# Kernel tuning notes

Measured on AMD Instinct MI355X. Metric: run time of the kernel, lower is better.

## Reference

```python
import jax, jax.numpy as jnp
import numpy as np

B, S, H = 2, 2048, 2048
E, I, TOPK = 8, 1408, 2


def setup_inputs() -> dict:
    key = jax.random.key(0)
    k0, k1, k2, k3, k4 = jax.random.split(key, 5)
    return {
        "hidden_states": jax.random.normal(k0, (B, S, H), dtype=jnp.float32),
        "Wr": jax.random.normal(k1, (H, E), dtype=jnp.float32) * 0.02,
        "Wg": jax.random.normal(k2, (E, H, I), dtype=jnp.float32) * 0.02,
        "Wu": jax.random.normal(k3, (E, H, I), dtype=jnp.float32) * 0.02,
        "Wd": jax.random.normal(k4, (E, I, H), dtype=jnp.float32) * 0.02,
    }


def reference(hidden_states, Wr, Wg, Wu, Wd):
    b, s, h = hidden_states.shape
    x = hidden_states.reshape(-1, h)                      # [T, H]
    T = x.shape[0]
    router_logits = x @ Wr                                # [T, E]
    probs = jax.nn.softmax(router_logits.astype(jnp.float32), axis=-1)
    top_w, top_i = jax.lax.top_k(probs, TOPK)             # [T, k]
    top_w = top_w / jnp.sum(top_w, axis=-1, keepdims=True)  # norm_topk_prob
    top_w = top_w.astype(x.dtype)
    # combine weights per (token, expert): zero where expert not selected
    cw = jnp.zeros((T, E), dtype=x.dtype).at[
        jnp.arange(T)[:, None], top_i].add(top_w)         # [T, E]
    # per-expert SwiGLU MLP computed densely, masked/weighted by cw
    g = jax.nn.silu(jnp.einsum('th,ehi->tei', x, Wg))     # [T, E, I]
    u = jnp.einsum('th,ehi->tei', x, Wu)                  # [T, E, I]
    y = jnp.einsum('tei,eih->teh', g * u, Wd)             # [T, E, H]
    out = jnp.einsum('te,teh->th', cw, y)                 # [T, H]
    return out.reshape(b, s, h), router_logits
```

## Files before the change

kernel.cpp:

```cpp
#include <hip/hip_runtime.h>

#define T_TOK 4096
#define HD 2048
#define NE 8
#define NI 1408

typedef __bf16 bf16x8 __attribute__((ext_vector_type(8)));
typedef float f32x4 __attribute__((ext_vector_type(4)));
typedef unsigned short ushort8 __attribute__((ext_vector_type(8)));

#define S_WAITCNT_VMCNT(n) asm volatile("s_waitcnt vmcnt(" #n ")" ::: "memory")
__device__ __forceinline__ void wave_barrier() {
  asm volatile("" ::: "memory");
  __builtin_amdgcn_s_barrier();
  asm volatile("" ::: "memory");
}

__device__ __forceinline__ unsigned short f2bf(float f) {
  unsigned int u = __float_as_uint(f);
  u += 0x7FFFu + ((u >> 16) & 1u);
  return (unsigned short)(u >> 16);
}
__device__ __forceinline__ float bf2f(unsigned short u) {
  return __uint_as_float((unsigned int)u << 16);
}

__device__ __forceinline__ void gload_lds16(const void* g, void* l) {
  __builtin_amdgcn_global_load_lds(
      (const __attribute__((address_space(1))) unsigned int*)g,
      (__attribute__((address_space(3))) unsigned int*)l, 16, 0, 0);
}

__global__ void transpose_cvt_kernel(const float* __restrict__ src,
                                     unsigned short* __restrict__ dst,
                                     int R, int C) {
  __shared__ float tile[64][65];
  int e = blockIdx.z;
  int r0 = blockIdx.y * 64, c0 = blockIdx.x * 64;
  const float* s = src + (size_t)e * R * C;
  unsigned short* d = dst + (size_t)e * R * C;
  int tid = threadIdx.x;
  int lr = tid >> 4, lc = (tid & 15) * 4;
#pragma unroll
  for (int p = 0; p < 4; p++) {
    int r = lr + p * 16;
    float4 v = *(const float4*)(s + (size_t)(r0 + r) * C + c0 + lc);
    tile[r][lc] = v.x; tile[r][lc + 1] = v.y;
    tile[r][lc + 2] = v.z; tile[r][lc + 3] = v.w;
  }
  __syncthreads();
  int rbase = (tid & 7) * 8, crel = tid >> 3;
#pragma unroll
  for (int p = 0; p < 2; p++) {
    int c = p * 32 + crel;
    ushort8 o;
#pragma unroll
    for (int j = 0; j < 8; j++) o[j] = f2bf(tile[rbase + j][c]);
    *(ushort8*)(d + (size_t)(c0 + c) * R + r0 + rbase) = o;
  }
}

__global__ void router_kernel(const float* __restrict__ x,
                              const float* __restrict__ Wr,
                              float* __restrict__ logits,
                              unsigned short* __restrict__ xbf,
                              int4* __restrict__ tokinfo,
                              int* __restrict__ cnt) {
  int wv = threadIdx.x >> 6, lane = threadIdx.x & 63;
  int t = blockIdx.x * 4 + wv;
  const float* xr = x + (size_t)t * HD;
  unsigned short* xbr = xbf + (size_t)t * HD;
  float acc[NE];
#pragma unroll
  for (int e = 0; e < NE; e++) acc[e] = 0.f;
  for (int hi = 0; hi < HD / 64; hi++) {
    int h = hi * 64 + lane;
    float xv = xr[h];
    xbr[h] = f2bf(xv);
    const float4* w4 = (const float4*)(Wr + (size_t)h * NE);
    float4 a = w4[0], b = w4[1];
    acc[0] += xv * a.x; acc[1] += xv * a.y; acc[2] += xv * a.z; acc[3] += xv * a.w;
    acc[4] += xv * b.x; acc[5] += xv * b.y; acc[6] += xv * b.z; acc[7] += xv * b.w;
  }
#pragma unroll
  for (int m = 32; m > 0; m >>= 1) {
#pragma unroll
    for (int e = 0; e < NE; e++) acc[e] += __shfl_xor(acc[e], m, 64);
  }
  if (lane < NE) logits[(size_t)t * NE + lane] = acc[lane];
  if (lane == 0) {
    int e0 = 0;
#pragma unroll
    for (int e = 1; e < NE; e++) if (acc[e] > acc[e0]) e0 = e;
    int e1 = (e0 == 0) ? 1 : 0;
#pragma unroll
    for (int e = 0; e < NE; e++) if (e != e0 && acc[e] > acc[e1]) e1 = e;
    float ex = expf(acc[e1] - acc[e0]);
    float w0 = 1.f / (1.f + ex);
    float w1 = ex / (1.f + ex);
    atomicAdd(&cnt[e0], 1);
    atomicAdd(&cnt[e1], 1);
    tokinfo[t] = make_int4(e0, e1, __float_as_int(w0), __float_as_int(w1));
  }
}

__global__ void offsets_kernel(int* __restrict__ cnt) {
  int o = 0;
  for (int e = 0; e < NE; e++) { cnt[8 + e] = o; o += cnt[e]; }
}

__global__ void scatter_kernel(const int4* __restrict__ tokinfo,
                               int* __restrict__ cnt,
                               int* __restrict__ row_tok,
                               int2* __restrict__ tok2row) {
  int t = blockIdx.x * blockDim.x + threadIdx.x;
  if (t >= T_TOK) return;
  int4 info = tokinfo[t];
  int p0 = atomicAdd(&cnt[16 + info.x], 1);
  int r0 = cnt[8 + info.x] + p0;
  row_tok[r0] = t;
  int p1 = atomicAdd(&cnt[16 + info.y], 1);
  int r1 = cnt[8 + info.y] + p1;
  row_tok[r1] = t;
  tok2row[t] = make_int2(r0, r1);
}

__launch_bounds__(256, 2)
__global__ void gemm1_kernel(const unsigned short* __restrict__ xbf,
                             const unsigned short* __restrict__ Wgt,
                             const unsigned short* __restrict__ Wut,
                             unsigned short* __restrict__ act,
                             const int* __restrict__ row_tok,
                             const int* __restrict__ cnt) {
  const int f = blockIdx.x + 11 * (blockIdx.y + 32 * blockIdx.z);
  const int e = f & 7;
  const int rem = f >> 3;
  const int nt = rem >> 5;
  const int mt = rem & 31;
  const int c = cnt[e];
  if (mt * 128 >= c) return;
  const int off = cnt[8 + e];
  const int rowbase = off + mt * 128, rowend = off + c;
  const int i0 = nt * 128;
  __shared__ __align__(16) char smem[49152];
  const int lane = threadIdx.x & 63, w = threadIdx.x >> 6;
  const int wr = w >> 1, wc = w & 1;

  const int rr0 = w * 16 + (lane >> 2);
  const int rr1 = rr0 + 64;
  const int q0 = (lane & 3) ^ ((rr0 >> 1) & 3);
  const int q1 = (lane & 3) ^ ((rr1 >> 1) & 3);
  int g0 = rowbase + rr0; if (g0 > rowend - 1) g0 = rowend - 1;
  int g1 = rowbase + rr1; if (g1 > rowend - 1) g1 = rowend - 1;
  const size_t tokA0 = (size_t)row_tok[g0] * HD;
  const size_t tokA1 = (size_t)row_tok[g1] * HD;
  const size_t bB0 = ((size_t)e * NI + i0 + rr0) * HD;
  const size_t bB1 = ((size_t)e * NI + i0 + rr1) * HD;
  const int ldsA = w * 1024;

  f32x4 zero = {0.f, 0.f, 0.f, 0.f};
  f32x4 accg[4][4], accu[4][4];
#pragma unroll
  for (int a = 0; a < 4; a++)
#pragma unroll
    for (int b = 0; b < 4; b++) { accg[a][b] = zero; accu[a][b] = zero; }

  auto stage = [&](int buf, int ks) {
    const int k0 = ks * 32;
    char* base = smem + buf * 24576;
    gload_lds16(xbf + tokA0 + k0 + q0 * 8, base + ldsA);
    gload_lds16(xbf + tokA1 + k0 + q1 * 8, base + ldsA + 4096);
    gload_lds16(Wgt + bB0 + k0 + q0 * 8, base + 8192 + ldsA);
    gload_lds16(Wgt + bB1 + k0 + q1 * 8, base + 8192 + ldsA + 4096);
    gload_lds16(Wut + bB0 + k0 + q0 * 8, base + 16384 + ldsA);
    gload_lds16(Wut + bB1 + k0 + q1 * 8, base + 16384 + ldsA + 4096);
  };
  const int rl = lane & 15, kslot = lane >> 4;
  auto compute = [&](int buf) {
    const char* base = smem + buf * 24576;
    bf16x8 af[4], bg[4], bu[4];
#pragma unroll
    for (int mi = 0; mi < 4; mi++) {
      int r = wr * 64 + mi * 16 + rl;
      int byt = r * 64 + ((kslot ^ ((r >> 1) & 3)) << 4);
      af[mi] = *(const bf16x8*)(base + byt);
    }
#pragma unroll
    for (int ni = 0; ni < 4; ni++) {
      int r = wc * 64 + ni * 16 + rl;
      int byt = r * 64 + ((kslot ^ ((r >> 1) & 3)) << 4);
      bg[ni] = *(const bf16x8*)(base + 8192 + byt);
      bu[ni] = *(const bf16x8*)(base + 16384 + byt);
    }
#pragma unroll
    for (int mi = 0; mi < 4; mi++)
#pragma unroll
      for (int ni = 0; ni < 4; ni++) {
        accg[mi][ni] = __builtin_amdgcn_mfma_f32_16x16x32_bf16(af[mi], bg[ni], accg[mi][ni], 0, 0, 0);
        accu[mi][ni] = __builtin_amdgcn_mfma_f32_16x16x32_bf16(af[mi], bu[ni], accu[mi][ni], 0, 0, 0);
      }
  };

  stage(0, 0);
  const int NKS = HD / 32;
  int ks = 0;
  for (; ks < NKS - 1; ks++) {
    stage((ks + 1) & 1, ks + 1);
    S_WAITCNT_VMCNT(6);
    wave_barrier();
    compute(ks & 1);
    wave_barrier();
  }
  S_WAITCNT_VMCNT(0);
  wave_barrier();
  compute(ks & 1);

  const int rh = lane >> 4;
#pragma unroll
  for (int mi = 0; mi < 4; mi++)
#pragma unroll
    for (int ni = 0; ni < 4; ni++)
#pragma unroll
      for (int j = 0; j < 4; j++) {
        int grow = rowbase + wr * 64 + mi * 16 + rh * 4 + j;
        if (grow < rowend) {
          int gcol = i0 + wc * 64 + ni * 16 + rl;
          float g = accg[mi][ni][j], u = accu[mi][ni][j];
          float val = g / (1.f + __expf(-g)) * u;
          act[(size_t)grow * NI + gcol] = f2bf(val);
        }
      }
}

__launch_bounds__(256, 3)
__global__ void gemm2_kernel(const unsigned short* __restrict__ act,
                             const unsigned short* __restrict__ Wdt,
                             unsigned short* __restrict__ y,
                             const int* __restrict__ cnt) {
  const int f = blockIdx.x + 16 * (blockIdx.y + 32 * blockIdx.z);
  const int e = f & 7;
  const int rem = f >> 3;
  const int nt = rem >> 5;
  const int mt = rem & 31;
  const int c = cnt[e];
  if (mt * 128 >= c) return;
  const int off = cnt[8 + e];
  const int rowbase = off + mt * 128, rowend = off + c;
  const int n0 = nt * 128;
  __shared__ __align__(16) char smem[32768];
  const int lane = threadIdx.x & 63, w = threadIdx.x >> 6;
  const int wr = w >> 1, wc = w & 1;

  const int rr0 = w * 16 + (lane >> 2);
  const int rr1 = rr0 + 64;
  const int q0 = (lane & 3) ^ ((rr0 >> 1) & 3);
  const int q1 = (lane & 3) ^ ((rr1 >> 1) & 3);
  int g0 = rowbase + rr0; if (g0 > rowend - 1) g0 = rowend - 1;
  int g1 = rowbase + rr1; if (g1 > rowend - 1) g1 = rowend - 1;
  const size_t aA0 = (size_t)g0 * NI;
  const size_t aA1 = (size_t)g1 * NI;
  const size_t bB0 = ((size_t)e * HD + n0 + rr0) * NI;
  const size_t bB1 = ((size_t)e * HD + n0 + rr1) * NI;
  const int ldsA = w * 1024;

  f32x4 zero = {0.f, 0.f, 0.f, 0.f};
  f32x4 acc[4][4];
#pragma unroll
  for (int a = 0; a < 4; a++)
#pragma unroll
    for (int b = 0; b < 4; b++) acc[a][b] = zero;

  auto stage = [&](int buf, int ks) {
    const int k0 = ks * 32;
    char* base = smem + buf * 16384;
    gload_lds16(act + aA0 + k0 + q0 * 8, base + ldsA);
    gload_lds16(act + aA1 + k0 + q1 * 8, base + ldsA + 4096);
    gload_lds16(Wdt + bB0 + k0 + q0 * 8, base + 8192 + ldsA);
    gload_lds16(Wdt + bB1 + k0 + q1 * 8, base + 8192 + ldsA + 4096);
  };
  const int rl = lane & 15, kslot = lane >> 4;
  auto compute = [&](int buf) {
    const char* base = smem + buf * 16384;
    bf16x8 af[4], bf[4];
#pragma unroll
    for (int mi = 0; mi < 4; mi++) {
      int r = wr * 64 + mi * 16 + rl;
      int byt = r * 64 + ((kslot ^ ((r >> 1) & 3)) << 4);
      af[mi] = *(const bf16x8*)(base + byt);
    }
#pragma unroll
    for (int ni = 0; ni < 4; ni++) {
      int r = wc * 64 + ni * 16 + rl;
      int byt = r * 64 + ((kslot ^ ((r >> 1) & 3)) << 4);
      bf[ni] = *(const bf16x8*)(base + 8192 + byt);
    }
#pragma unroll
    for (int mi = 0; mi < 4; mi++)
#pragma unroll
      for (int ni = 0; ni < 4; ni++)
        acc[mi][ni] = __builtin_amdgcn_mfma_f32_16x16x32_bf16(af[mi], bf[ni], acc[mi][ni], 0, 0, 0);
  };

  stage(0, 0);
  const int NKS = NI / 32;
  int ks = 0;
  for (; ks < NKS - 1; ks++) {
    stage((ks + 1) & 1, ks + 1);
    S_WAITCNT_VMCNT(4);
    wave_barrier();
    compute(ks & 1);
    wave_barrier();
  }
  S_WAITCNT_VMCNT(0);
  wave_barrier();
  compute(ks & 1);

  const int rh = lane >> 4;
#pragma unroll
  for (int mi = 0; mi < 4; mi++)
#pragma unroll
    for (int ni = 0; ni < 4; ni++)
#pragma unroll
      for (int j = 0; j < 4; j++) {
        int grow = rowbase + wr * 64 + mi * 16 + rh * 4 + j;
        if (grow < rowend) {
          int gcol = n0 + wc * 64 + ni * 16 + rl;
          y[(size_t)grow * HD + gcol] = f2bf(acc[mi][ni][j]);
        }
      }
}

__global__ void combine_kernel(const unsigned short* __restrict__ y,
                               const int2* __restrict__ tok2row,
                               const int4* __restrict__ tokinfo,
                               float* __restrict__ out) {
  int t = blockIdx.x, tid = threadIdx.x;
  int2 rr = tok2row[t];
  int4 info = tokinfo[t];
  float w0 = __int_as_float(info.z), w1 = __int_as_float(info.w);
  ushort8 a = ((const ushort8*)(y + (size_t)rr.x * HD))[tid];
  ushort8 b = ((const ushort8*)(y + (size_t)rr.y * HD))[tid];
  float4 o0, o1;
  o0.x = w0 * bf2f(a[0]) + w1 * bf2f(b[0]);
  o0.y = w0 * bf2f(a[1]) + w1 * bf2f(b[1]);
  o0.z = w0 * bf2f(a[2]) + w1 * bf2f(b[2]);
  o0.w = w0 * bf2f(a[3]) + w1 * bf2f(b[3]);
  o1.x = w0 * bf2f(a[4]) + w1 * bf2f(b[4]);
  o1.y = w0 * bf2f(a[5]) + w1 * bf2f(b[5]);
  o1.z = w0 * bf2f(a[6]) + w1 * bf2f(b[6]);
  o1.w = w0 * bf2f(a[7]) + w1 * bf2f(b[7]);
  float4* op = (float4*)(out + (size_t)t * HD + tid * 8);
  op[0] = o0; op[1] = o1;
}

extern "C" void kernel_launch(void* const* d_in, const int* in_sizes, int n_in,
                              void* d_out, int out_size, void* d_ws, size_t ws_size,
                              hipStream_t stream) {
  const float* x  = (const float*)d_in[0];
  const float* Wr = (const float*)d_in[1];
  const float* Wg = (const float*)d_in[2];
  const float* Wu = (const float*)d_in[3];
  const float* Wd = (const float*)d_in[4];
  float* out = (float*)d_out;
  char* ws = (char*)d_ws;

  unsigned short* xbf = (unsigned short*)(ws);
  unsigned short* Wgt = (unsigned short*)(ws + 16777216);
  unsigned short* Wut = (unsigned short*)(ws + 62914560);
  unsigned short* Wdt = (unsigned short*)(ws + 109051904);
  unsigned short* act = (unsigned short*)(ws + 155189248);
  unsigned short* yb  = (unsigned short*)(ws + 16777216);
  int4*  tokinfo      = (int4*)(ws + 178257920);
  int*   row_tok      = (int*)(ws + 178323456);
  int2*  tok2row      = (int2*)(ws + 178356224);
  int*   cnt          = (int*)(ws + 178388992);

  hipMemsetAsync(cnt, 0, 96, stream);

  router_kernel<<<T_TOK / 4, 256, 0, stream>>>(x, Wr, out + (size_t)T_TOK * HD, xbf, tokinfo, cnt);
  offsets_kernel<<<1, 1, 0, stream>>>(cnt);
  scatter_kernel<<<T_TOK / 256, 256, 0, stream>>>(tokinfo, cnt, row_tok, tok2row);

  transpose_cvt_kernel<<<dim3(NI / 64, HD / 64, NE), 256, 0, stream>>>(Wg, Wgt, HD, NI);
  transpose_cvt_kernel<<<dim3(NI / 64, HD / 64, NE), 256, 0, stream>>>(Wu, Wut, HD, NI);
  transpose_cvt_kernel<<<dim3(HD / 64, NI / 64, NE), 256, 0, stream>>>(Wd, Wdt, NI, HD);

  gemm1_kernel<<<dim3(11, 32, NE), 256, 0, stream>>>(xbf, Wgt, Wut, act, row_tok, cnt);
  gemm2_kernel<<<dim3(16, 32, NE), 256, 0, stream>>>(act, Wdt, yb, cnt);
  combine_kernel<<<T_TOK, 256, 0, stream>>>(yb, tok2row, tokinfo, out);
}
```

Baseline: 459.9 us.

## Switch expert GEMMs to 32x32x16 MFMA and merge Wg/Wu transpose launches

Both expert GEMM kernels move from 16x16x32 MFMA tiles to 32x32x16 MFMA with 16-wide accumulators. LDS fragment loads and the epilogue row/column mapping are rewritten to match, and s_setprio is raised around the MFMA block. The larger instruction is meant to cut LDS reads per FLOP and raise matrix-core throughput. The Wg and Wu transpose-convert launches are also merged into one kernel, removing a launch. The epilogue index math must match the 32x32 output layout or results will be wrong.

```diff
diff --git a/kernel.cpp b/kernel.cpp
--- a/kernel.cpp
+++ b/kernel.cpp
@@ -7,6 +7,7 @@
 
 typedef __bf16 bf16x8 __attribute__((ext_vector_type(8)));
 typedef float f32x4 __attribute__((ext_vector_type(4)));
+typedef float f32x16 __attribute__((ext_vector_type(16)));
 typedef unsigned short ushort8 __attribute__((ext_vector_type(8)));
 
 #define S_WAITCNT_VMCNT(n) asm volatile("s_waitcnt vmcnt(" #n ")" ::: "memory")
@@ -31,14 +32,19 @@
       (__attribute__((address_space(3))) unsigned int*)l, 16, 0, 0);
 }
 
-__global__ void transpose_cvt_kernel(const float* __restrict__ src,
-                                     unsigned short* __restrict__ dst,
-                                     int R, int C) {
+__global__ void transpose_cvt2_kernel(const float* __restrict__ srcA,
+                                      unsigned short* __restrict__ dstA,
+                                      const float* __restrict__ srcB,
+                                      unsigned short* __restrict__ dstB,
+                                      int R, int C, int dual) {
   __shared__ float tile[64][65];
-  int e = blockIdx.z;
+  int z = blockIdx.z;
+  int e = dual ? (z >> 1) : z;
+  const float* sp = (dual && (z & 1)) ? srcB : srcA;
+  unsigned short* dp = (dual && (z & 1)) ? dstB : dstA;
   int r0 = blockIdx.y * 64, c0 = blockIdx.x * 64;
-  const float* s = src + (size_t)e * R * C;
-  unsigned short* d = dst + (size_t)e * R * C;
+  const float* s = sp + (size_t)e * R * C;
+  unsigned short* d = dp + (size_t)e * R * C;
   int tid = threadIdx.x;
   int lr = tid >> 4, lc = (tid & 15) * 4;
 #pragma unroll
@@ -158,12 +164,14 @@
   const size_t bB1 = ((size_t)e * NI + i0 + rr1) * HD;
   const int ldsA = w * 1024;
 
-  f32x4 zero = {0.f, 0.f, 0.f, 0.f};
-  f32x4 accg[4][4], accu[4][4];
-#pragma unroll
-  for (int a = 0; a < 4; a++)
-#pragma unroll
-    for (int b = 0; b < 4; b++) { accg[a][b] = zero; accu[a][b] = zero; }
+  f32x16 accg[2][2], accu[2][2];
+#pragma unroll
+  for (int a = 0; a < 2; a++)
+#pragma unroll
+    for (int b = 0; b < 2; b++) {
+      accg[a][b] = (f32x16)(0.f);
+      accu[a][b] = (f32x16)(0.f);
+    }
 
   auto stage = [&](int buf, int ks) {
     const int k0 = ks * 32;
@@ -175,30 +183,40 @@
     gload_lds16(Wut + bB0 + k0 + q0 * 8, base + 16384 + ldsA);
     gload_lds16(Wut + bB1 + k0 + q1 * 8, base + 16384 + ldsA + 4096);
   };
-  const int rl = lane & 15, kslot = lane >> 4;
+  const int rl32 = lane & 31, khalf = lane >> 5;
   auto compute = [&](int buf) {
     const char* base = smem + buf * 24576;
-    bf16x8 af[4], bg[4], bu[4];
-#pragma unroll
-    for (int mi = 0; mi < 4; mi++) {
-      int r = wr * 64 + mi * 16 + rl;
-      int byt = r * 64 + ((kslot ^ ((r >> 1) & 3)) << 4);
-      af[mi] = *(const bf16x8*)(base + byt);
-    }
-#pragma unroll
-    for (int ni = 0; ni < 4; ni++) {
-      int r = wc * 64 + ni * 16 + rl;
-      int byt = r * 64 + ((kslot ^ ((r >> 1) & 3)) << 4);
-      bg[ni] = *(const bf16x8*)(base + 8192 + byt);
-      bu[ni] = *(const bf16x8*)(base + 16384 + byt);
-    }
-#pragma unroll
-    for (int mi = 0; mi < 4; mi++)
-#pragma unroll
-      for (int ni = 0; ni < 4; ni++) {
-        accg[mi][ni] = __builtin_amdgcn_mfma_f32_16x16x32_bf16(af[mi], bg[ni], accg[mi][ni], 0, 0, 0);
-        accu[mi][ni] = __builtin_amdgcn_mfma_f32_16x16x32_bf16(af[mi], bu[ni], accu[mi][ni], 0, 0, 0);
-      }
+    bf16x8 af[2][2], bg[2][2], bu[2][2];
+#pragma unroll
+    for (int mi = 0; mi < 2; mi++)
+#pragma unroll
+      for (int s = 0; s < 2; s++) {
+        int r = wr * 64 + mi * 32 + rl32;
+        int slot = (2 * s + khalf) ^ ((r >> 1) & 3);
+        af[mi][s] = *(const bf16x8*)(base + r * 64 + slot * 16);
+      }
+#pragma unroll
+    for (int ni = 0; ni < 2; ni++)
+#pragma unroll
+      for (int s = 0; s < 2; s++) {
+        int r = wc * 64 + ni * 32 + rl32;
+        int slot = (2 * s + khalf) ^ ((r >> 1) & 3);
+        bg[ni][s] = *(const bf16x8*)(base + 8192 + r * 64 + slot * 16);
+        bu[ni][s] = *(const bf16x8*)(base + 16384 + r * 64 + slot * 16);
+      }
+    __builtin_amdgcn_s_setprio(1);
+#pragma unroll
+    for (int s = 0; s < 2; s++)
+#pragma unroll
+      for (int mi = 0; mi < 2; mi++)
+#pragma unroll
+        for (int ni = 0; ni < 2; ni++) {
+          accg[mi][ni] = __builtin_amdgcn_mfma_f32_32x32x16_bf16(
+              af[mi][s], bg[ni][s], accg[mi][ni], 0, 0, 0);
+          accu[mi][ni] = __builtin_amdgcn_mfma_f32_32x32x16_bf16(
+              af[mi][s], bu[ni][s], accu[mi][ni], 0, 0, 0);
+        }
+    __builtin_amdgcn_s_setprio(0);
   };
 
   stage(0, 0);
@@ -215,16 +233,15 @@
   wave_barrier();
   compute(ks & 1);
 
-  const int rh = lane >> 4;
-#pragma unroll
-  for (int mi = 0; mi < 4; mi++)
-#pragma unroll
-    for (int ni = 0; ni < 4; ni++)
-#pragma unroll
-      for (int j = 0; j < 4; j++) {
-        int grow = rowbase + wr * 64 + mi * 16 + rh * 4 + j;
+#pragma unroll
+  for (int mi = 0; mi < 2; mi++)
+#pragma unroll
+    for (int ni = 0; ni < 2; ni++)
+#pragma unroll
+      for (int j = 0; j < 16; j++) {
+        int grow = rowbase + wr * 64 + mi * 32 + (j & 3) + 8 * (j >> 2) + 4 * khalf;
         if (grow < rowend) {
-          int gcol = i0 + wc * 64 + ni * 16 + rl;
+          int gcol = i0 + wc * 64 + ni * 32 + rl32;
           float g = accg[mi][ni][j], u = accu[mi][ni][j];
           float val = g / (1.f + __expf(-g)) * u;
           act[(size_t)grow * NI + gcol] = f2bf(val);
@@ -263,12 +280,11 @@
   const size_t bB1 = ((size_t)e * HD + n0 + rr1) * NI;
   const int ldsA = w * 1024;
 
-  f32x4 zero = {0.f, 0.f, 0.f, 0.f};
-  f32x4 acc[4][4];
-#pragma unroll
-  for (int a = 0; a < 4; a++)
-#pragma unroll
-    for (int b = 0; b < 4; b++) acc[a][b] = zero;
+  f32x16 acc[2][2];
+#pragma unroll
+  for (int a = 0; a < 2; a++)
+#pragma unroll
+    for (int b = 0; b < 2; b++) acc[a][b] = (f32x16)(0.f);
 
   auto stage = [&](int buf, int ks) {
     const int k0 = ks * 32;
@@ -278,27 +294,36 @@
     gload_lds16(Wdt + bB0 + k0 + q0 * 8, base + 8192 + ldsA);
     gload_lds16(Wdt + bB1 + k0 + q1 * 8, base + 8192 + ldsA + 4096);
   };
-  const int rl = lane & 15, kslot = lane >> 4;
+  const int rl32 = lane & 31, khalf = lane >> 5;
   auto compute = [&](int buf) {
     const char* base = smem + buf * 16384;
-    bf16x8 af[4], bf[4];
-#pragma unroll
-    for (int mi = 0; mi < 4; mi++) {
-      int r = wr * 64 + mi * 16 + rl;
-      int byt = r * 64 + ((kslot ^ ((r >> 1) & 3)) << 4);
-      af[mi] = *(const bf16x8*)(base + byt);
-    }
-#pragma unroll
-    for (int ni = 0; ni < 4; ni++) {
-      int r = wc * 64 + ni * 16 + rl;
-      int byt = r * 64 + ((kslot ^ ((r >> 1) & 3)) << 4);
-      bf[ni] = *(const bf16x8*)(base + 8192 + byt);
-    }
-#pragma unroll
-    for (int mi = 0; mi < 4; mi++)
-#pragma unroll
-      for (int ni = 0; ni < 4; ni++)
-        acc[mi][ni] = __builtin_amdgcn_mfma_f32_16x16x32_bf16(af[mi], bf[ni], acc[mi][ni], 0, 0, 0);
+    bf16x8 af[2][2], bf[2][2];
+#pragma unroll
+    for (int mi = 0; mi < 2; mi++)
+#pragma unroll
+      for (int s = 0; s < 2; s++) {
+        int r = wr * 64 + mi * 32 + rl32;
+        int slot = (2 * s + khalf) ^ ((r >> 1) & 3);
+        af[mi][s] = *(const bf16x8*)(base + r * 64 + slot * 16);
+      }
+#pragma unroll
+    for (int ni = 0; ni < 2; ni++)
+#pragma unroll
+      for (int s = 0; s < 2; s++) {
+        int r = wc * 64 + ni * 32 + rl32;
+        int slot = (2 * s + khalf) ^ ((r >> 1) & 3);
+        bf[ni][s] = *(const bf16x8*)(base + 8192 + r * 64 + slot * 16);
+      }
+    __builtin_amdgcn_s_setprio(1);
+#pragma unroll
+    for (int s = 0; s < 2; s++)
+#pragma unroll
+      for (int mi = 0; mi < 2; mi++)
+#pragma unroll
+        for (int ni = 0; ni < 2; ni++)
+          acc[mi][ni] = __builtin_amdgcn_mfma_f32_32x32x16_bf16(
+              af[mi][s], bf[ni][s], acc[mi][ni], 0, 0, 0);
+    __builtin_amdgcn_s_setprio(0);
   };
 
   stage(0, 0);
@@ -315,16 +340,15 @@
   wave_barrier();
   compute(ks & 1);
 
-  const int rh = lane >> 4;
-#pragma unroll
-  for (int mi = 0; mi < 4; mi++)
-#pragma unroll
-    for (int ni = 0; ni < 4; ni++)
-#pragma unroll
-      for (int j = 0; j < 4; j++) {
-        int grow = rowbase + wr * 64 + mi * 16 + rh * 4 + j;
+#pragma unroll
+  for (int mi = 0; mi < 2; mi++)
+#pragma unroll
+    for (int ni = 0; ni < 2; ni++)
+#pragma unroll
+      for (int j = 0; j < 16; j++) {
+        int grow = rowbase + wr * 64 + mi * 32 + (j & 3) + 8 * (j >> 2) + 4 * khalf;
         if (grow < rowend) {
-          int gcol = n0 + wc * 64 + ni * 16 + rl;
+          int gcol = n0 + wc * 64 + ni * 32 + rl32;
           y[(size_t)grow * HD + gcol] = f2bf(acc[mi][ni][j]);
         }
       }
@@ -381,9 +405,10 @@
   offsets_kernel<<<1, 1, 0, stream>>>(cnt);
   scatter_kernel<<<T_TOK / 256, 256, 0, stream>>>(tokinfo, cnt, row_tok, tok2row);
 
-  transpose_cvt_kernel<<<dim3(NI / 64, HD / 64, NE), 256, 0, stream>>>(Wg, Wgt, HD, NI);
-  transpose_cvt_kernel<<<dim3(NI / 64, HD / 64, NE), 256, 0, stream>>>(Wu, Wut, HD, NI);
-  transpose_cvt_kernel<<<dim3(HD / 64, NI / 64, NE), 256, 0, stream>>>(Wd, Wdt, NI, HD);
+  transpose_cvt2_kernel<<<dim3(NI / 64, HD / 64, NE * 2), 256, 0, stream>>>(
+      Wg, Wgt, Wu, Wut, HD, NI, 1);
+  transpose_cvt2_kernel<<<dim3(HD / 64, NI / 64, NE), 256, 0, stream>>>(
+      Wd, Wdt, nullptr, nullptr, NI, HD, 0);
 
   gemm1_kernel<<<dim3(11, 32, NE), 256, 0, stream>>>(xbf, Wgt, Wut, act, row_tok, cnt);
   gemm2_kernel<<<dim3(16, 32, NE), 256, 0, stream>>>(act, Wdt, yb, cnt);
```

New measurement: 488.0 us. +6.1%, slower.

## Fuse weight transpose and bf16 conversion into GEMM B-tile loading

Applied to the files above, without the earlier changes.

Removes the three separate transpose/convert kernels for Wg, Wu and Wd. The GEMM kernels now read the fp32 weights directly into registers, convert them to bf16 and write them transposed and swizzled into LDS. The pipeline is restructured so the register loads for the next k-step overlap the current MFMA compute. This avoids a full extra read and write pass over the weights, but each GEMM block now re-reads fp32 weights, which doubles their bytes and repeats the load across M tiles. It also adds VALU conversion work and LDS store traffic inside the main loop.

```diff
diff --git a/kernel.cpp b/kernel.cpp
--- a/kernel.cpp
+++ b/kernel.cpp
@@ -6,10 +6,12 @@
 #define NI 1408
 
 typedef __bf16 bf16x8 __attribute__((ext_vector_type(8)));
+typedef __bf16 bf16x4 __attribute__((ext_vector_type(4)));
 typedef float f32x4 __attribute__((ext_vector_type(4)));
 typedef unsigned short ushort8 __attribute__((ext_vector_type(8)));
 
 #define S_WAITCNT_VMCNT(n) asm volatile("s_waitcnt vmcnt(" #n ")" ::: "memory")
+#define S_WAITCNT_LGKM0() asm volatile("s_waitcnt lgkmcnt(0)" ::: "memory")
 __device__ __forceinline__ void wave_barrier() {
   asm volatile("" ::: "memory");
   __builtin_amdgcn_s_barrier();
@@ -29,35 +31,6 @@
   __builtin_amdgcn_global_load_lds(
       (const __attribute__((address_space(1))) unsigned int*)g,
       (__attribute__((address_space(3))) unsigned int*)l, 16, 0, 0);
-}
-
-__global__ void transpose_cvt_kernel(const float* __restrict__ src,
-                                     unsigned short* __restrict__ dst,
-                                     int R, int C) {
-  __shared__ float tile[64][65];
-  int e = blockIdx.z;
-  int r0 = blockIdx.y * 64, c0 = blockIdx.x * 64;
-  const float* s = src + (size_t)e * R * C;
-  unsigned short* d = dst + (size_t)e * R * C;
-  int tid = threadIdx.x;
-  int lr = tid >> 4, lc = (tid & 15) * 4;
-#pragma unroll
-  for (int p = 0; p < 4; p++) {
-    int r = lr + p * 16;
-    float4 v = *(const float4*)(s + (size_t)(r0 + r) * C + c0 + lc);
-    tile[r][lc] = v.x; tile[r][lc + 1] = v.y;
-    tile[r][lc + 2] = v.z; tile[r][lc + 3] = v.w;
-  }
-  __syncthreads();
-  int rbase = (tid & 7) * 8, crel = tid >> 3;
-#pragma unroll
-  for (int p = 0; p < 2; p++) {
-    int c = p * 32 + crel;
-    ushort8 o;
-#pragma unroll
-    for (int j = 0; j < 8; j++) o[j] = f2bf(tile[rbase + j][c]);
-    *(ushort8*)(d + (size_t)(c0 + c) * R + r0 + rbase) = o;
-  }
 }
 
 __global__ void router_kernel(const float* __restrict__ x,
@@ -127,8 +100,8 @@
 
 __launch_bounds__(256, 2)
 __global__ void gemm1_kernel(const unsigned short* __restrict__ xbf,
-                             const unsigned short* __restrict__ Wgt,
-                             const unsigned short* __restrict__ Wut,
+                             const float* __restrict__ Wg,
+                             const float* __restrict__ Wu,
                              unsigned short* __restrict__ act,
                              const int* __restrict__ row_tok,
                              const int* __restrict__ cnt) {
@@ -143,7 +116,8 @@
   const int rowbase = off + mt * 128, rowend = off + c;
   const int i0 = nt * 128;
   __shared__ __align__(16) char smem[49152];
-  const int lane = threadIdx.x & 63, w = threadIdx.x >> 6;
+  const int tid = threadIdx.x;
+  const int lane = tid & 63, w = tid >> 6;
   const int wr = w >> 1, wc = w & 1;
 
   const int rr0 = w * 16 + (lane >> 2);
@@ -154,9 +128,14 @@
   int g1 = rowbase + rr1; if (g1 > rowend - 1) g1 = rowend - 1;
   const size_t tokA0 = (size_t)row_tok[g0] * HD;
   const size_t tokA1 = (size_t)row_tok[g1] * HD;
-  const size_t bB0 = ((size_t)e * NI + i0 + rr0) * HD;
-  const size_t bB1 = ((size_t)e * NI + i0 + rr1) * HD;
   const int ldsA = w * 1024;
+
+  const int bm = tid >> 7;
+  const int bt = tid & 127;
+  const int bc = (bt & 31) * 4;
+  const int bo = bt >> 5;
+  const float* Wsel = (bm ? Wu : Wg) + (size_t)e * HD * NI + (i0 + bc);
+  const int ldsB = 8192 + bm * 8192;
 
   f32x4 zero = {0.f, 0.f, 0.f, 0.f};
   f32x4 accg[4][4], accu[4][4];
@@ -165,16 +144,31 @@
 #pragma unroll
     for (int b = 0; b < 4; b++) { accg[a][b] = zero; accu[a][b] = zero; }
 
-  auto stage = [&](int buf, int ks) {
+  f32x4 breg[8];
+  auto loadB = [&](int ks) {
+    const float* src = Wsel + (size_t)(ks * 32 + bo * 8) * NI;
+#pragma unroll
+    for (int j = 0; j < 8; j++)
+      breg[j] = *(const f32x4*)(src + (size_t)j * NI);
+  };
+  auto writeB = [&](int buf) {
+    char* base = smem + buf * 24576 + ldsB;
+#pragma unroll
+    for (int ci = 0; ci < 4; ci++) {
+      int n = bc + ci;
+      bf16x8 v;
+#pragma unroll
+      for (int j = 0; j < 8; j++) v[j] = (__bf16)breg[j][ci];
+      *(bf16x8*)(base + n * 64 + ((bo ^ ((n >> 1) & 3)) << 4)) = v;
+    }
+  };
+  auto stageA = [&](int buf, int ks) {
     const int k0 = ks * 32;
     char* base = smem + buf * 24576;
     gload_lds16(xbf + tokA0 + k0 + q0 * 8, base + ldsA);
     gload_lds16(xbf + tokA1 + k0 + q1 * 8, base + ldsA + 4096);
-    gload_lds16(Wgt + bB0 + k0 + q0 * 8, base + 8192 + ldsA);
-    gload_lds16(Wgt + bB1 + k0 + q1 * 8, base + 8192 + ldsA + 4096);
-    gload_lds16(Wut + bB0 + k0 + q0 * 8, base + 16384 + ldsA);
-    gload_lds16(Wut + bB1 + k0 + q1 * 8, base + 16384 + ldsA + 4096);
-  };
+  };
+
   const int rl = lane & 15, kslot = lane >> 4;
   auto compute = [&](int buf) {
     const char* base = smem + buf * 24576;
@@ -201,19 +195,29 @@
       }
   };
 
-  stage(0, 0);
+  loadB(0);
+  stageA(0, 0);
+  S_WAITCNT_VMCNT(0);
+  writeB(0);
+  S_WAITCNT_LGKM0();
+  wave_barrier();
+
   const int NKS = HD / 32;
-  int ks = 0;
-  for (; ks < NKS - 1; ks++) {
-    stage((ks + 1) & 1, ks + 1);
-    S_WAITCNT_VMCNT(6);
-    wave_barrier();
-    compute(ks & 1);
-    wave_barrier();
+  for (int ks = 0; ks < NKS; ks++) {
+    const int cur = ks & 1;
+    if (ks + 1 < NKS) {
+      loadB(ks + 1);
+      stageA(cur ^ 1, ks + 1);
+      S_WAITCNT_VMCNT(2);
+      writeB(cur ^ 1);
+      compute(cur);
+      S_WAITCNT_VMCNT(0);
+      S_WAITCNT_LGKM0();
+      wave_barrier();
+    } else {
+      compute(cur);
+    }
   }
-  S_WAITCNT_VMCNT(0);
-  wave_barrier();
-  compute(ks & 1);
 
   const int rh = lane >> 4;
 #pragma unroll
@@ -234,7 +238,7 @@
 
 __launch_bounds__(256, 3)
 __global__ void gemm2_kernel(const unsigned short* __restrict__ act,
-                             const unsigned short* __restrict__ Wdt,
+                             const float* __restrict__ Wd,
                              unsigned short* __restrict__ y,
                              const int* __restrict__ cnt) {
   const int f = blockIdx.x + 16 * (blockIdx.y + 32 * blockIdx.z);
@@ -248,7 +252,8 @@
   const int rowbase = off + mt * 128, rowend = off + c;
   const int n0 = nt * 128;
   __shared__ __align__(16) char smem[32768];
-  const int lane = threadIdx.x & 63, w = threadIdx.x >> 6;
+  const int tid = threadIdx.x;
+  const int lane = tid & 63, w = tid >> 6;
   const int wr = w >> 1, wc = w & 1;
 
   const int rr0 = w * 16 + (lane >> 2);
@@ -259,9 +264,11 @@
   int g1 = rowbase + rr1; if (g1 > rowend - 1) g1 = rowend - 1;
   const size_t aA0 = (size_t)g0 * NI;
   const size_t aA1 = (size_t)g1 * NI;
-  const size_t bB0 = ((size_t)e * HD + n0 + rr0) * NI;
-  const size_t bB1 = ((size_t)e * HD + n0 + rr1) * NI;
   const int ldsA = w * 1024;
+
+  const int bc = (tid & 31) * 4;
+  const int bq = tid >> 5;
+  const float* Wsel = Wd + (size_t)e * NI * HD + (n0 + bc);
 
   f32x4 zero = {0.f, 0.f, 0.f, 0.f};
   f32x4 acc[4][4];
@@ -270,14 +277,32 @@
 #pragma unroll
     for (int b = 0; b < 4; b++) acc[a][b] = zero;
 
-  auto stage = [&](int buf, int ks) {
+  f32x4 breg[4];
+  auto loadB = [&](int ks) {
+    const float* src = Wsel + (size_t)(ks * 32 + bq * 4) * HD;
+#pragma unroll
+    for (int j = 0; j < 4; j++)
+      breg[j] = *(const f32x4*)(src + (size_t)j * HD);
+  };
+  auto writeB = [&](int buf) {
+    char* base = smem + buf * 16384 + 8192;
+    const int o = bq >> 1, half = bq & 1;
+#pragma unroll
+    for (int ci = 0; ci < 4; ci++) {
+      int n = bc + ci;
+      bf16x4 v;
+#pragma unroll
+      for (int j = 0; j < 4; j++) v[j] = (__bf16)breg[j][ci];
+      *(bf16x4*)(base + n * 64 + ((o ^ ((n >> 1) & 3)) << 4) + half * 8) = v;
+    }
+  };
+  auto stageA = [&](int buf, int ks) {
     const int k0 = ks * 32;
     char* base = smem + buf * 16384;
     gload_lds16(act + aA0 + k0 + q0 * 8, base + ldsA);
     gload_lds16(act + aA1 + k0 + q1 * 8, base + ldsA + 4096);
-    gload_lds16(Wdt + bB0 + k0 + q0 * 8, base + 8192 + ldsA);
-    gload_lds16(Wdt + bB1 + k0 + q1 * 8, base + 8192 + ldsA + 4096);
-  };
+  };
+
   const int rl = lane & 15, kslot = lane >> 4;
   auto compute = [&](int buf) {
     const char* base = smem + buf * 16384;
@@ -301,19 +326,29 @@
         acc[mi][ni] = __builtin_amdgcn_mfma_f32_16x16x32_bf16(af[mi], bf[ni], acc[mi][ni], 0, 0, 0);
   };
 
-  stage(0, 0);
+  loadB(0);
+  stageA(0, 0);
+  S_WAITCNT_VMCNT(0);
+  writeB(0);
+  S_WAITCNT_LGKM0();
+  wave_barrier();
+
   const int NKS = NI / 32;
-  int ks = 0;
-  for (; ks < NKS - 1; ks++) {
-    stage((ks + 1) & 1, ks + 1);
-    S_WAITCNT_VMCNT(4);
-    wave_barrier();
-    compute(ks & 1);
-    wave_barrier();
+  for (int ks = 0; ks < NKS; ks++) {
+    const int cur = ks & 1;
+    if (ks + 1 < NKS) {
+      loadB(ks + 1);
+      stageA(cur ^ 1, ks + 1);
+      S_WAITCNT_VMCNT(2);
+      writeB(cur ^ 1);
+      compute(cur);
+      S_WAITCNT_VMCNT(0);
+      S_WAITCNT_LGKM0();
+      wave_barrier();
+    } else {
+      compute(cur);
+    }
   }
-  S_WAITCNT_VMCNT(0);
-  wave_barrier();
-  compute(ks & 1);
 
   const int rh = lane >> 4;
 #pragma unroll
@@ -365,15 +400,12 @@
   char* ws = (char*)d_ws;
 
   unsigned short* xbf = (unsigned short*)(ws);
-  unsigned short* Wgt = (unsigned short*)(ws + 16777216);
-  unsigned short* Wut = (unsigned short*)(ws + 62914560);
-  unsigned short* Wdt = (unsigned short*)(ws + 109051904);
-  unsigned short* act = (unsigned short*)(ws + 155189248);
-  unsigned short* yb  = (unsigned short*)(ws + 16777216);
-  int4*  tokinfo      = (int4*)(ws + 178257920);
-  int*   row_tok      = (int*)(ws + 178323456);
-  int2*  tok2row      = (int2*)(ws + 178356224);
-  int*   cnt          = (int*)(ws + 178388992);
+  unsigned short* act = (unsigned short*)(ws + 16777216);
+  unsigned short* yb  = (unsigned short*)(ws + 39845888);
+  int4*  tokinfo      = (int4*)(ws + 73400320);
+  int*   row_tok      = (int*)(ws + 73465856);
+  int2*  tok2row      = (int2*)(ws + 73498624);
+  int*   cnt          = (int*)(ws + 73531392);
 
   hipMemsetAsync(cnt, 0, 96, stream);
 
@@ -381,11 +413,7 @@
   offsets_kernel<<<1, 1, 0, stream>>>(cnt);
   scatter_kernel<<<T_TOK / 256, 256, 0, stream>>>(tokinfo, cnt, row_tok, tok2row);
 
-  transpose_cvt_kernel<<<dim3(NI / 64, HD / 64, NE), 256, 0, stream>>>(Wg, Wgt, HD, NI);
-  transpose_cvt_kernel<<<dim3(NI / 64, HD / 64, NE), 256, 0, stream>>>(Wu, Wut, HD, NI);
-  transpose_cvt_kernel<<<dim3(HD / 64, NI / 64, NE), 256, 0, stream>>>(Wd, Wdt, NI, HD);
-
-  gemm1_kernel<<<dim3(11, 32, NE), 256, 0, stream>>>(xbf, Wgt, Wut, act, row_tok, cnt);
-  gemm2_kernel<<<dim3(16, 32, NE), 256, 0, stream>>>(act, Wdt, yb, cnt);
+  gemm1_kernel<<<dim3(11, 32, NE), 256, 0, stream>>>(xbf, Wg, Wu, act, row_tok, cnt);
+  gemm2_kernel<<<dim3(16, 32, NE), 256, 0, stream>>>(act, Wd, yb, cnt);
   combine_kernel<<<T_TOK, 256, 0, stream>>>(yb, tok2row, tokinfo, out);
 }
```

New measurement: 595.4 us. 1.29x slower.

## Use persistent work-list scheduling for MoE grouped GEMMs and merge weight transposes

Applied to the files above, without the earlier changes.

The offsets kernel now builds a compact list of (expert, m-tile) pairs. Both grouped GEMMs become persistent kernels that fetch tiles from that list through a global atomic counter, instead of launching a full dense grid where most blocks exit early. The gate and up weight transposes are merged into one launch, and gemm2's launch bounds go from 3 to 4 blocks. This removes idle early-exit blocks and launch overhead, but adds a per-tile atomic and __syncthreads, and the extra occupancy may cost registers.

```diff
diff --git a/kernel.cpp b/kernel.cpp
--- a/kernel.cpp
+++ b/kernel.cpp
@@ -31,14 +31,19 @@
       (__attribute__((address_space(3))) unsigned int*)l, 16, 0, 0);
 }
 
-__global__ void transpose_cvt_kernel(const float* __restrict__ src,
-                                     unsigned short* __restrict__ dst,
-                                     int R, int C) {
+__global__ void transpose_cvt2_kernel(const float* __restrict__ srcA,
+                                      unsigned short* __restrict__ dstA,
+                                      const float* __restrict__ srcB,
+                                      unsigned short* __restrict__ dstB,
+                                      int R, int C, int dual) {
   __shared__ float tile[64][65];
-  int e = blockIdx.z;
+  int z = blockIdx.z;
+  int e = dual ? (z >> 1) : z;
+  const float* sp = (dual && (z & 1)) ? srcB : srcA;
+  unsigned short* dp = (dual && (z & 1)) ? dstB : dstA;
   int r0 = blockIdx.y * 64, c0 = blockIdx.x * 64;
-  const float* s = src + (size_t)e * R * C;
-  unsigned short* d = dst + (size_t)e * R * C;
+  const float* s = sp + (size_t)e * R * C;
+  unsigned short* d = dp + (size_t)e * R * C;
   int tid = threadIdx.x;
   int lr = tid >> 4, lc = (tid & 15) * 4;
 #pragma unroll
@@ -104,9 +109,16 @@
   }
 }
 
-__global__ void offsets_kernel(int* __restrict__ cnt) {
-  int o = 0;
-  for (int e = 0; e < NE; e++) { cnt[8 + e] = o; o += cnt[e]; }
+__global__ void offsets_kernel(int* __restrict__ cnt, int* __restrict__ wl) {
+  int o = 0, n = 0;
+  for (int e = 0; e < NE; e++) {
+    cnt[8 + e] = o;
+    int c = cnt[e];
+    o += c;
+    int mts = (c + 127) >> 7;
+    for (int mt = 0; mt < mts; mt++) wl[n++] = (e << 16) | mt;
+  }
+  cnt[24] = n;
 }
 
 __global__ void scatter_kernel(const int4* __restrict__ tokinfo,
@@ -131,203 +143,221 @@
                              const unsigned short* __restrict__ Wut,
                              unsigned short* __restrict__ act,
                              const int* __restrict__ row_tok,
-                             const int* __restrict__ cnt) {
-  const int f = blockIdx.x + 11 * (blockIdx.y + 32 * blockIdx.z);
-  const int e = f & 7;
-  const int rem = f >> 3;
-  const int nt = rem >> 5;
-  const int mt = rem & 31;
-  const int c = cnt[e];
-  if (mt * 128 >= c) return;
-  const int off = cnt[8 + e];
-  const int rowbase = off + mt * 128, rowend = off + c;
-  const int i0 = nt * 128;
+                             int* __restrict__ cnt,
+                             const int* __restrict__ wl) {
   __shared__ __align__(16) char smem[49152];
-  const int lane = threadIdx.x & 63, w = threadIdx.x >> 6;
+  __shared__ int sidx;
+  const int tid = threadIdx.x;
+  const int lane = tid & 63, w = tid >> 6;
   const int wr = w >> 1, wc = w & 1;
-
+  const int nwl = cnt[24];
+  const int total = nwl * (NI / 128);
+  const int ldsA = w * 1024;
+  const int rl = lane & 15, kslot = lane >> 4;
   const int rr0 = w * 16 + (lane >> 2);
   const int rr1 = rr0 + 64;
   const int q0 = (lane & 3) ^ ((rr0 >> 1) & 3);
   const int q1 = (lane & 3) ^ ((rr1 >> 1) & 3);
-  int g0 = rowbase + rr0; if (g0 > rowend - 1) g0 = rowend - 1;
-  int g1 = rowbase + rr1; if (g1 > rowend - 1) g1 = rowend - 1;
-  const size_t tokA0 = (size_t)row_tok[g0] * HD;
-  const size_t tokA1 = (size_t)row_tok[g1] * HD;
-  const size_t bB0 = ((size_t)e * NI + i0 + rr0) * HD;
-  const size_t bB1 = ((size_t)e * NI + i0 + rr1) * HD;
-  const int ldsA = w * 1024;
-
-  f32x4 zero = {0.f, 0.f, 0.f, 0.f};
-  f32x4 accg[4][4], accu[4][4];
-#pragma unroll
-  for (int a = 0; a < 4; a++)
-#pragma unroll
-    for (int b = 0; b < 4; b++) { accg[a][b] = zero; accu[a][b] = zero; }
-
-  auto stage = [&](int buf, int ks) {
-    const int k0 = ks * 32;
-    char* base = smem + buf * 24576;
-    gload_lds16(xbf + tokA0 + k0 + q0 * 8, base + ldsA);
-    gload_lds16(xbf + tokA1 + k0 + q1 * 8, base + ldsA + 4096);
-    gload_lds16(Wgt + bB0 + k0 + q0 * 8, base + 8192 + ldsA);
-    gload_lds16(Wgt + bB1 + k0 + q1 * 8, base + 8192 + ldsA + 4096);
-    gload_lds16(Wut + bB0 + k0 + q0 * 8, base + 16384 + ldsA);
-    gload_lds16(Wut + bB1 + k0 + q1 * 8, base + 16384 + ldsA + 4096);
-  };
-  const int rl = lane & 15, kslot = lane >> 4;
-  auto compute = [&](int buf) {
-    const char* base = smem + buf * 24576;
-    bf16x8 af[4], bg[4], bu[4];
-#pragma unroll
-    for (int mi = 0; mi < 4; mi++) {
-      int r = wr * 64 + mi * 16 + rl;
-      int byt = r * 64 + ((kslot ^ ((r >> 1) & 3)) << 4);
-      af[mi] = *(const bf16x8*)(base + byt);
+
+  for (;;) {
+    if (tid == 0) sidx = atomicAdd(&cnt[25], 1);
+    __syncthreads();
+    const int idx = sidx;
+    if (idx >= total) break;
+    const int nt = idx / nwl;
+    const int went = wl[idx - nt * nwl];
+    const int e = went >> 16, mt = went & 0xffff;
+    const int c = cnt[e];
+    const int off = cnt[8 + e];
+    const int rowbase = off + mt * 128, rowend = off + c;
+    const int i0 = nt * 128;
+
+    int g0 = rowbase + rr0; if (g0 > rowend - 1) g0 = rowend - 1;
+    int g1 = rowbase + rr1; if (g1 > rowend - 1) g1 = rowend - 1;
+    const size_t tokA0 = (size_t)row_tok[g0] * HD;
+    const size_t tokA1 = (size_t)row_tok[g1] * HD;
+    const size_t bB0 = ((size_t)e * NI + i0 + rr0) * HD;
+    const size_t bB1 = ((size_t)e * NI + i0 + rr1) * HD;
+
+    f32x4 zero = {0.f, 0.f, 0.f, 0.f};
+    f32x4 accg[4][4], accu[4][4];
+#pragma unroll
+    for (int a = 0; a < 4; a++)
+#pragma unroll
+      for (int b = 0; b < 4; b++) { accg[a][b] = zero; accu[a][b] = zero; }
+
+    auto stage = [&](int buf, int ks) {
+      const int k0 = ks * 32;
+      char* base = smem + buf * 24576;
+      gload_lds16(xbf + tokA0 + k0 + q0 * 8, base + ldsA);
+      gload_lds16(xbf + tokA1 + k0 + q1 * 8, base + ldsA + 4096);
+      gload_lds16(Wgt + bB0 + k0 + q0 * 8, base + 8192 + ldsA);
+      gload_lds16(Wgt + bB1 + k0 + q1 * 8, base + 8192 + ldsA + 4096);
+      gload_lds16(Wut + bB0 + k0 + q0 * 8, base + 16384 + ldsA);
+      gload_lds16(Wut + bB1 + k0 + q1 * 8, base + 16384 + ldsA + 4096);
+    };
+    auto compute = [&](int buf) {
+      const char* base = smem + buf * 24576;
+      bf16x8 af[4], bg[4], bu[4];
+#pragma unroll
+      for (int mi = 0; mi < 4; mi++) {
+        int r = wr * 64 + mi * 16 + rl;
+        int byt = r * 64 + ((kslot ^ ((r >> 1) & 3)) << 4);
+        af[mi] = *(const bf16x8*)(base + byt);
+      }
+#pragma unroll
+      for (int ni = 0; ni < 4; ni++) {
+        int r = wc * 64 + ni * 16 + rl;
+        int byt = r * 64 + ((kslot ^ ((r >> 1) & 3)) << 4);
+        bg[ni] = *(const bf16x8*)(base + 8192 + byt);
+        bu[ni] = *(const bf16x8*)(base + 16384 + byt);
+      }
+#pragma unroll
+      for (int mi = 0; mi < 4; mi++)
+#pragma unroll
+        for (int ni = 0; ni < 4; ni++) {
+          accg[mi][ni] = __builtin_amdgcn_mfma_f32_16x16x32_bf16(af[mi], bg[ni], accg[mi][ni], 0, 0, 0);
+          accu[mi][ni] = __builtin_amdgcn_mfma_f32_16x16x32_bf16(af[mi], bu[ni], accu[mi][ni], 0, 0, 0);
+        }
+    };
+
+    stage(0, 0);
+    const int NKS = HD / 32;
+    int ks = 0;
+    for (; ks < NKS - 1; ks++) {
+      stage((ks + 1) & 1, ks + 1);
+      S_WAITCNT_VMCNT(6);
+      wave_barrier();
+      compute(ks & 1);
+      wave_barrier();
     }
-#pragma unroll
-    for (int ni = 0; ni < 4; ni++) {
-      int r = wc * 64 + ni * 16 + rl;
-      int byt = r * 64 + ((kslot ^ ((r >> 1) & 3)) << 4);
-      bg[ni] = *(const bf16x8*)(base + 8192 + byt);
-      bu[ni] = *(const bf16x8*)(base + 16384 + byt);
-    }
-#pragma unroll
-    for (int mi = 0; mi < 4; mi++)
-#pragma unroll
-      for (int ni = 0; ni < 4; ni++) {
-        accg[mi][ni] = __builtin_amdgcn_mfma_f32_16x16x32_bf16(af[mi], bg[ni], accg[mi][ni], 0, 0, 0);
-        accu[mi][ni] = __builtin_amdgcn_mfma_f32_16x16x32_bf16(af[mi], bu[ni], accu[mi][ni], 0, 0, 0);
-      }
-  };
-
-  stage(0, 0);
-  const int NKS = HD / 32;
-  int ks = 0;
-  for (; ks < NKS - 1; ks++) {
-    stage((ks + 1) & 1, ks + 1);
-    S_WAITCNT_VMCNT(6);
+    S_WAITCNT_VMCNT(0);
     wave_barrier();
     compute(ks & 1);
-    wave_barrier();
-  }
-  S_WAITCNT_VMCNT(0);
-  wave_barrier();
-  compute(ks & 1);
-
-  const int rh = lane >> 4;
-#pragma unroll
-  for (int mi = 0; mi < 4; mi++)
-#pragma unroll
-    for (int ni = 0; ni < 4; ni++)
-#pragma unroll
-      for (int j = 0; j < 4; j++) {
-        int grow = rowbase + wr * 64 + mi * 16 + rh * 4 + j;
-        if (grow < rowend) {
-          int gcol = i0 + wc * 64 + ni * 16 + rl;
-          float g = accg[mi][ni][j], u = accu[mi][ni][j];
-          float val = g / (1.f + __expf(-g)) * u;
-          act[(size_t)grow * NI + gcol] = f2bf(val);
+
+    const int rh = lane >> 4;
+#pragma unroll
+    for (int mi = 0; mi < 4; mi++)
+#pragma unroll
+      for (int ni = 0; ni < 4; ni++)
+#pragma unroll
+        for (int j = 0; j < 4; j++) {
+          int grow = rowbase + wr * 64 + mi * 16 + rh * 4 + j;
+          if (grow < rowend) {
+            int gcol = i0 + wc * 64 + ni * 16 + rl;
+            float g = accg[mi][ni][j], u = accu[mi][ni][j];
+            float val = g / (1.f + __expf(-g)) * u;
+            act[(size_t)grow * NI + gcol] = f2bf(val);
+          }
         }
-      }
-}
-
-__launch_bounds__(256, 3)
+  }
+}
+
+__launch_bounds__(256, 4)
 __global__ void gemm2_kernel(const unsigned short* __restrict__ act,
                              const unsigned short* __restrict__ Wdt,
                              unsigned short* __restrict__ y,
-                             const int* __restrict__ cnt) {
-  const int f = blockIdx.x + 16 * (blockIdx.y + 32 * blockIdx.z);
-  const int e = f & 7;
-  const int rem = f >> 3;
-  const int nt = rem >> 5;
-  const int mt = rem & 31;
-  const int c = cnt[e];
-  if (mt * 128 >= c) return;
-  const int off = cnt[8 + e];
-  const int rowbase = off + mt * 128, rowend = off + c;
-  const int n0 = nt * 128;
+                             int* __restrict__ cnt,
+                             const int* __restrict__ wl) {
   __shared__ __align__(16) char smem[32768];
-  const int lane = threadIdx.x & 63, w = threadIdx.x >> 6;
+  __shared__ int sidx;
+  const int tid = threadIdx.x;
+  const int lane = tid & 63, w = tid >> 6;
   const int wr = w >> 1, wc = w & 1;
-
+  const int nwl = cnt[24];
+  const int total = nwl * (HD / 128);
+  const int ldsA = w * 1024;
+  const int rl = lane & 15, kslot = lane >> 4;
   const int rr0 = w * 16 + (lane >> 2);
   const int rr1 = rr0 + 64;
   const int q0 = (lane & 3) ^ ((rr0 >> 1) & 3);
   const int q1 = (lane & 3) ^ ((rr1 >> 1) & 3);
-  int g0 = rowbase + rr0; if (g0 > rowend - 1) g0 = rowend - 1;
-  int g1 = rowbase + rr1; if (g1 > rowend - 1) g1 = rowend - 1;
-  const size_t aA0 = (size_t)g0 * NI;
-  const size_t aA1 = (size_t)g1 * NI;
-  const size_t bB0 = ((size_t)e * HD + n0 + rr0) * NI;
-  const size_t bB1 = ((size_t)e * HD + n0 + rr1) * NI;
-  const int ldsA = w * 1024;
-
-  f32x4 zero = {0.f, 0.f, 0.f, 0.f};
-  f32x4 acc[4][4];
-#pragma unroll
-  for (int a = 0; a < 4; a++)
-#pragma unroll
-    for (int b = 0; b < 4; b++) acc[a][b] = zero;
-
-  auto stage = [&](int buf, int ks) {
-    const int k0 = ks * 32;
-    char* base = smem + buf * 16384;
-    gload_lds16(act + aA0 + k0 + q0 * 8, base + ldsA);
-    gload_lds16(act + aA1 + k0 + q1 * 8, base + ldsA + 4096);
-    gload_lds16(Wdt + bB0 + k0 + q0 * 8, base + 8192 + ldsA);
-    gload_lds16(Wdt + bB1 + k0 + q1 * 8, base + 8192 + ldsA + 4096);
-  };
-  const int rl = lane & 15, kslot = lane >> 4;
-  auto compute = [&](int buf) {
-    const char* base = smem + buf * 16384;
-    bf16x8 af[4], bf[4];
-#pragma unroll
-    for (int mi = 0; mi < 4; mi++) {
-      int r = wr * 64 + mi * 16 + rl;
-      int byt = r * 64 + ((kslot ^ ((r >> 1) & 3)) << 4);
-      af[mi] = *(const bf16x8*)(base + byt);
+
+  for (;;) {
+    if (tid == 0) sidx = atomicAdd(&cnt[26], 1);
+    __syncthreads();
+    const int idx = sidx;
+    if (idx >= total) break;
+    const int nt = idx / nwl;
+    const int went = wl[idx - nt * nwl];
+    const int e = went >> 16, mt = went & 0xffff;
+    const int c = cnt[e];
+    const int off = cnt[8 + e];
+    const int rowbase = off + mt * 128, rowend = off + c;
+    const int n0 = nt * 128;
+
+    int g0 = rowbase + rr0; if (g0 > rowend - 1) g0 = rowend - 1;
+    int g1 = rowbase + rr1; if (g1 > rowend - 1) g1 = rowend - 1;
+    const size_t aA0 = (size_t)g0 * NI;
+    const size_t aA1 = (size_t)g1 * NI;
+    const size_t bB0 = ((size_t)e * HD + n0 + rr0) * NI;
+    const size_t bB1 = ((size_t)e * HD + n0 + rr1) * NI;
+
+    f32x4 zero = {0.f, 0.f, 0.f, 0.f};
+    f32x4 acc[4][4];
+#pragma unroll
+    for (int a = 0; a < 4; a++)
+#pragma unroll
+      for (int b = 0; b < 4; b++) acc[a][b] = zero;
+
+    auto stage = [&](int buf, int ks) {
+      const int k0 = ks * 32;
+      char* base = smem + buf * 16384;
+      gload_lds16(act + aA0 + k0 + q0 * 8, base + ldsA);
+      gload_lds16(act + aA1 + k0 + q1 * 8, base + ldsA + 4096);
+      gload_lds16(Wdt + bB0 + k0 + q0 * 8, base + 8192 + ldsA);
+      gload_lds16(Wdt + bB1 + k0 + q1 * 8, base + 8192 + ldsA + 4096);
+    };
+    auto compute = [&](int buf) {
+      const char* base = smem + buf * 16384;
+      bf16x8 af[4], bf[4];
+#pragma unroll
+      for (int mi = 0; mi < 4; mi++) {
+        int r = wr * 64 + mi * 16 + rl;
+        int byt = r * 64 + ((kslot ^ ((r >> 1) & 3)) << 4);
+        af[mi] = *(const bf16x8*)(base + byt);
+      }
+#pragma unroll
+      for (int ni = 0; ni < 4; ni++) {
+        int r = wc * 64 + ni * 16 + rl;
+        int byt = r * 64 + ((kslot ^ ((r >> 1) & 3)) << 4);
+        bf[ni] = *(const bf16x8*)(base + 8192 + byt);
+      }
+#pragma unroll
+      for (int mi = 0; mi < 4; mi++)
+#pragma unroll
+        for (int ni = 0; ni < 4; ni++)
+          acc[mi][ni] = __builtin_amdgcn_mfma_f32_16x16x32_bf16(af[mi], bf[ni], acc[mi][ni], 0, 0, 0);
+    };
+
+    stage(0, 0);
+    const int NKS = NI / 32;
+    int ks = 0;
+    for (; ks < NKS - 1; ks++) {
+      stage((ks + 1) & 1, ks + 1);
+      S_WAITCNT_VMCNT(4);
+      wave_barrier();
+      compute(ks & 1);
+      wave_barrier();
     }
-#pragma unroll
-    for (int ni = 0; ni < 4; ni++) {
-      int r = wc * 64 + ni * 16 + rl;
-      int byt = r * 64 + ((kslot ^ ((r >> 1) & 3)) << 4);
-      bf[ni] = *(const bf16x8*)(base + 8192 + byt);
-    }
-#pragma unroll
-    for (int mi = 0; mi < 4; mi++)
-#pragma unroll
-      for (int ni = 0; ni < 4; ni++)
-        acc[mi][ni] = __builtin_amdgcn_mfma_f32_16x16x32_bf16(af[mi], bf[ni], acc[mi][ni], 0, 0, 0);
-  };
-
-  stage(0, 0);
-  const int NKS = NI / 32;
-  int ks = 0;
-  for (; ks < NKS - 1; ks++) {
-    stage((ks + 1) & 1, ks + 1);
-    S_WAITCNT_VMCNT(4);
+    S_WAITCNT_VMCNT(0);
     wave_barrier();
     compute(ks & 1);
-    wave_barrier();
-  }
-  S_WAITCNT_VMCNT(0);
-  wave_barrier();
-  compute(ks & 1);
-
-  const int rh = lane >> 4;
-#pragma unroll
-  for (int mi = 0; mi < 4; mi++)
-#pragma unroll
-    for (int ni = 0; ni < 4; ni++)
-#pragma unroll
-      for (int j = 0; j < 4; j++) {
-        int grow = rowbase + wr * 64 + mi * 16 + rh * 4 + j;
-        if (grow < rowend) {
-          int gcol = n0 + wc * 64 + ni * 16 + rl;
-          y[(size_t)grow * HD + gcol] = f2bf(acc[mi][ni][j]);
+
+    const int rh = lane >> 4;
+#pragma unroll
+    for (int mi = 0; mi < 4; mi++)
+#pragma unroll
+      for (int ni = 0; ni < 4; ni++)
+#pragma unroll
+        for (int j = 0; j < 4; j++) {
+          int grow = rowbase + wr * 64 + mi * 16 + rh * 4 + j;
+          if (grow < rowend) {
+            int gcol = n0 + wc * 64 + ni * 16 + rl;
+            y[(size_t)grow * HD + gcol] = f2bf(acc[mi][ni][j]);
+          }
         }
-      }
+  }
 }
 
 __global__ void combine_kernel(const unsigned short* __restrict__ y,
@@ -374,18 +404,20 @@
   int*   row_tok      = (int*)(ws + 178323456);
   int2*  tok2row      = (int2*)(ws + 178356224);
   int*   cnt          = (int*)(ws + 178388992);
-
-  hipMemsetAsync(cnt, 0, 96, stream);
+  int*   wl           = (int*)(ws + 178389120);
+
+  hipMemsetAsync(cnt, 0, 128, stream);
 
   router_kernel<<<T_TOK / 4, 256, 0, stream>>>(x, Wr, out + (size_t)T_TOK * HD, xbf, tokinfo, cnt);
-  offsets_kernel<<<1, 1, 0, stream>>>(cnt);
+  offsets_kernel<<<1, 1, 0, stream>>>(cnt, wl);
   scatter_kernel<<<T_TOK / 256, 256, 0, stream>>>(tokinfo, cnt, row_tok, tok2row);
 
-  transpose_cvt_kernel<<<dim3(NI / 64, HD / 64, NE), 256, 0, stream>>>(Wg, Wgt, HD, NI);
-  transpose_cvt_kernel<<<dim3(NI / 64, HD / 64, NE), 256, 0, stream>>>(Wu, Wut, HD, NI);
-  transpose_cvt_kernel<<<dim3(HD / 64, NI / 64, NE), 256, 0, stream>>>(Wd, Wdt, NI, HD);
-
-  gemm1_kernel<<<dim3(11, 32, NE), 256, 0, stream>>>(xbf, Wgt, Wut, act, row_tok, cnt);
-  gemm2_kernel<<<dim3(16, 32, NE), 256, 0, stream>>>(act, Wdt, yb, cnt);
+  transpose_cvt2_kernel<<<dim3(NI / 64, HD / 64, NE * 2), 256, 0, stream>>>(
+      Wg, Wgt, Wu, Wut, HD, NI, 1);
+  transpose_cvt2_kernel<<<dim3(HD / 64, NI / 64, NE), 256, 0, stream>>>(
+      Wd, Wdt, nullptr, nullptr, NI, HD, 0);
+
+  gemm1_kernel<<<512, 256, 0, stream>>>(xbf, Wgt, Wut, act, row_tok, cnt, wl);
+  gemm2_kernel<<<1024, 256, 0, stream>>>(act, Wdt, yb, cnt, wl);
   combine_kernel<<<T_TOK, 256, 0, stream>>>(yb, tok2row, tokinfo, out);
 }
```

New measurement: 519.0 us. 12.8% more time.
